# Kernel tuning notes

Hardware: AMD Instinct MI355X
Metric: run time of the kernel (lower is better)

Reference implementation:

```python
import jax, jax.numpy as jnp
import numpy as np

B, N, D, H = 16384, 64, 64, 128
DECAY_W = 2.0  # Decayer(2, 'rev') -> 1 / (1 + w * dt)
EPS = 1e-12


def setup_inputs() -> dict:
    key = jax.random.key(0)
    ks = jax.random.split(key, 16)
    return {
        "dt_node": jax.random.uniform(ks[0], (B,)) * 10.0,
        "deg_node": jax.random.uniform(ks[1], (B,)),
        "cc_node": jax.random.uniform(ks[2], (B,)),
        "dt_neigh": jax.random.uniform(ks[3], (B, N)) * 10.0,
        "deg_neigh": jax.random.uniform(ks[4], (B, N)),
        "cc_neigh": jax.random.uniform(ks[5], (B, N)),
        "neigh_mask": jax.random.bernoulli(ks[6], 0.7, (B, N)),
        "feature_hist": jax.random.normal(ks[7], (B, 2 * D)),
        "t2v_w": jax.random.normal(ks[8], (D,)) * 0.1,
        "t2v_b": jax.random.normal(ks[9], (D,)) * 0.1,
        "node_w": jax.random.normal(ks[10], (D,)) * 0.1,
        "node_b": jax.random.normal(ks[11], (D,)) * 0.1,
        "att_W1": jax.random.normal(ks[12], (D, D)) * (1.0 / np.sqrt(D)),
        "att_W2": jax.random.normal(ks[13], (D, D)) * (1.0 / np.sqrt(D)),
        "att_v": jax.random.normal(ks[14], (D,)) * (1.0 / np.sqrt(D)),
        "weight": jax.random.normal(ks[15], (H, 4 * D)) * (1.0 / np.sqrt(4 * D)),
    }


def _time2vec(t, w, b):
    # Time2Vec('cos'): first channel linear, rest cos-activated. t: [...], -> [..., D]
    v = t[..., None] * w + b
    return jnp.concatenate([v[..., :1], jnp.cos(v[..., 1:])], axis=-1)


def _node_feat(dt, deg, cc, t2v_w, t2v_b, node_w, node_b):
    # linear_node(deg) + linear_node(cc) + time2vec(|dt|), then L2 normalize
    f = (_time2vec(jnp.abs(dt), t2v_w, t2v_b)
         + (deg[..., None] * node_w + node_b)
         + (cc[..., None] * node_w + node_b))
    nrm = jnp.maximum(jnp.linalg.norm(f, axis=-1, keepdims=True), EPS)
    return f / nrm


def reference(dt_node, deg_node, cc_node, dt_neigh, deg_neigh, cc_neigh,
              neigh_mask, feature_hist, t2v_w, t2v_b, node_w, node_b,
              att_W1, att_W2, att_v, weight):
    node_f = _node_feat(dt_node, deg_node, cc_node, t2v_w, t2v_b, node_w, node_b)      # [B, D]
    neigh_f = _node_feat(dt_neigh, deg_neigh, cc_neigh, t2v_w, t2v_b, node_w, node_b)  # [B, N, D]

    # temporal decay: Decayer(2, 'rev')
    time_score = 1.0 / (1.0 + DECAY_W * dt_neigh)                                       # [B, N]

    h = jnp.tanh((node_f @ att_W1)[:, None, :] + jnp.einsum('bnd,de->bne', neigh_f, att_W2))
    att = jnp.einsum('bne,e->bn', h, att_v)                                             # [B, N]

    score = jax.nn.leaky_relu(time_score) * att                                         # [B, N]
    m = neigh_mask.astype(node_f.dtype)
    n_in = jnp.maximum(jnp.sum(m, axis=-1, keepdims=True), 1.0)                         # [B, 1]
    w_n = (m * score) / n_in                                                            # [B, N]
    neigh_agg = jnp.einsum('bn,bnd->bd', w_n, neigh_f)                                  # [B, D]

    combined = jnp.concatenate([node_f, neigh_agg, feature_hist], axis=-1)              # [B, 4D]
    return jax.nn.relu(combined @ weight.T)                                             # [B, H]
```

## Files before the change

### kernel.cpp

```cpp
#include <hip/hip_runtime.h>
#include <hip/hip_bf16.h>

#define B_SZ 16384
#define N_SZ 64
#define D_SZ 64
#define H_SZ 128
#define R_PB 4
#define ARS 68
#define CRS 264

typedef short bf16x8 __attribute__((ext_vector_type(8)));
typedef float f32x4  __attribute__((ext_vector_type(4)));
typedef float f32x2  __attribute__((ext_vector_type(2)));

__device__ __forceinline__ float bflo(unsigned u){union{unsigned i;float f;}c;c.i=u<<16;return c.f;}
__device__ __forceinline__ float bits2f(unsigned short r){union{unsigned i;float f;}c;c.i=((unsigned)r)<<16;return c.f;}
__device__ __forceinline__ unsigned f2bfbits(float f){
    __hip_bfloat16 h = __float2bfloat16(f);
    unsigned short u;
    __builtin_memcpy(&u, &h, 2);
    return (unsigned)u;
}
__device__ __forceinline__ unsigned pack2bf(float a, float b){
    __hip_bfloat162 h = __float22bfloat162_rn(make_float2(a, b));
    unsigned r;
    __builtin_memcpy(&r, &h, 4);
    return r;
}
__device__ __forceinline__ float bf2f(__hip_bfloat16 x) { return __bfloat162float(x); }

template<int CTRL>
__device__ __forceinline__ float dpp_add(float v){
    int t = __builtin_amdgcn_mov_dpp(__builtin_bit_cast(int, v), CTRL, 0xf, 0xf, true);
    return v + __builtin_bit_cast(float, t);
}

__device__ __forceinline__ float tanh_fast(float x){
    float e = __expf(2.0f * x);
    return 1.0f - __fdividef(2.0f, e + 1.0f);
}

template<int FMODE>
__device__ __forceinline__ float LD(const void* p, int i) {
    if constexpr (FMODE == 0) return bf2f(((const __hip_bfloat16*)p)[i]);
    else                      return ((const float*)p)[i];
}

__device__ __forceinline__ float mval(const void* p, int i, int mode) {
    if (mode == 0) return ((const int*)p)[i]            ? 1.0f : 0.0f;
    if (mode == 1) return ((const unsigned char*)p)[i]  ? 1.0f : 0.0f;
    if (mode == 2) return ((const unsigned short*)p)[i] ? 1.0f : 0.0f;
    return ((const unsigned int*)p)[i]                  ? 1.0f : 0.0f;
}

__device__ __forceinline__ int detect_f32(const void* p) {
    const uint4* q = (const uint4*)p;
    unsigned o = 0;
    #pragma unroll
    for (int i = 0; i < 8; ++i) { uint4 v = q[i]; o |= v.x | v.y | v.z | v.w; }
    return (o & 0x80008000u) ? 1 : 0;
}

__device__ __forceinline__ int detect_mask_mode(const void* p) {
    const uint4* q = (const uint4*)p;
    unsigned oa = 0, ofe = 0;
    #pragma unroll
    for (int i = 0; i < 8; ++i) {
        uint4 v = q[i];
        unsigned w = v.x | v.y | v.z | v.w;
        oa  |= w;
        ofe |= (v.x & 0xFEFEFEFEu) | (v.y & 0xFEFEFEFEu) | (v.z & 0xFEFEFEFEu) | (v.w & 0xFEFEFEFEu);
    }
    if ((oa & 0xFFFFFF00u) == 0) return 0;
    if (ofe == 0)                return 1;
    if (oa & 0x000000FEu)        return 2;
    return 3;
}

__global__ void prep_kernel(const void* dt_node, const void* att_W1, const void* att_W2,
                            void* ws) {
    const int t     = blockIdx.x * 256 + threadIdx.x;
    const int fmode = detect_f32(dt_node);
    const int fi  = t >> 6, ln = t & 63;
    const int et  = fi >> 2, ks = fi & 3;
    const int m16 = ln & 15, qd = ln >> 4;
    const int col = et * 16 + m16;
    unsigned short s[8];
    #pragma unroll
    for (int j = 0; j < 8; ++j) {
        const int i = ks * 32 + qd * 8 + j;
        if (fmode == 0) {
            s[j] = (i < 64) ? ((const unsigned short*)att_W1)[i * D_SZ + col]
                            : ((const unsigned short*)att_W2)[(i - 64) * D_SZ + col];
        } else {
            const float v = (i < 64) ? ((const float*)att_W1)[i * D_SZ + col]
                                     : ((const float*)att_W2)[(i - 64) * D_SZ + col];
            s[j] = (unsigned short)f2bfbits(v);
        }
    }
    ((uint4*)ws)[t] = make_uint4(((unsigned)s[0]) | (((unsigned)s[1]) << 16),
                                 ((unsigned)s[2]) | (((unsigned)s[3]) << 16),
                                 ((unsigned)s[4]) | (((unsigned)s[5]) << 16),
                                 ((unsigned)s[6]) | (((unsigned)s[7]) << 16));
}

struct Smem {
    alignas(16) unsigned short A[R_PB * 65 * ARS];
    alignas(16) unsigned short comb[R_PB * CRS];
    alignas(16) float prm[4][D_SZ];
    float att[R_PB][N_SZ];
    float wn[R_PB][N_SZ];
};

__device__ __forceinline__ void feat_row(float t, float dc,
                                         const float* sw, const float* sb,
                                         const float* snw, const float* snb,
                                         int c, unsigned short* dstA, unsigned short* dstC) {
    f32x2 fp[8]; float ss = 0.0f;
    #pragma unroll
    for (int g = 0; g < 8; ++g) {
        const f32x2 w  = *(const f32x2*)(sw  + 2 * g);
        const f32x2 b  = *(const f32x2*)(sb  + 2 * g);
        const f32x2 nw = *(const f32x2*)(snw + 2 * g);
        const f32x2 nb = *(const f32x2*)(snb + 2 * g);
        f32x2 v = w * t + b;
        f32x2 cv;
        cv.x = (c == 0 && g == 0) ? v.x : __cosf(v.x);
        cv.y = __cosf(v.y);
        f32x2 f = cv + (nw * dc + nb);
        ss = fmaf(f.x, f.x, ss);
        ss = fmaf(f.y, f.y, ss);
        fp[g] = f;
    }
    ss += __shfl_xor(ss, 1, 4);
    ss += __shfl_xor(ss, 2, 4);
    const float inv = 1.0f / fmaxf(sqrtf(ss), 1e-12f);
    unsigned pk[8];
    #pragma unroll
    for (int g = 0; g < 8; ++g)
        pk[g] = pack2bf(fp[g].x * inv, fp[g].y * inv);
    uint4 v0 = make_uint4(pk[0], pk[1], pk[2], pk[3]);
    uint4 v1 = make_uint4(pk[4], pk[5], pk[6], pk[7]);
    ((uint4*)dstA)[0] = v0; ((uint4*)dstA)[1] = v1;
    if (dstC) { ((uint4*)dstC)[0] = v0; ((uint4*)dstC)[1] = v1; }
}

template<int FMODE, bool USE_WS>
__device__ __forceinline__ void body(
    Smem& sm,
    const void* dt_node, const void* deg_node, const void* cc_node,
    const void* dt_neigh, const void* deg_neigh, const void* cc_neigh,
    const void* neigh_mask, const void* feature_hist,
    const void* t2v_w, const void* t2v_b, const void* node_w, const void* node_b,
    const void* att_W1, const void* att_W2, const void* att_v,
    const void* weight, void* out, const void* ws, int mmode, int b0, int tid)
{
    const int lane = tid & 63;
    const int wv   = tid >> 6;
    const int m16  = lane & 15;
    const int quad = lane >> 4;

    {
        const int arr = tid >> 6, ch = tid & 63;
        float v;
        if      (arr == 0) v = LD<FMODE>(t2v_w,  ch);
        else if (arr == 1) v = LD<FMODE>(t2v_b,  ch);
        else if (arr == 2) v = LD<FMODE>(node_w, ch);
        else               v = 2.0f * LD<FMODE>(node_b, ch);
        sm.prm[arr][ch] = v;
    }
    __syncthreads();

    {
        const int c = tid & 3, d0 = c * 16;
        const float* sw  = sm.prm[0] + d0;
        const float* sb  = sm.prm[1] + d0;
        const float* snw = sm.prm[2] + d0;
        const float* snb = sm.prm[3] + d0;

        #pragma unroll
        for (int it = 0; it < 5; ++it) {
            const int t = tid + it * 256;
            if (t < R_PB * 65 * 4) {
                const int f = t >> 2;
                if (f < R_PB * 64) {
                    const int row = f >> 6, n = f & 63;
                    const int idx = (b0 + row) * N_SZ + n;
                    const float tn  = fabsf(LD<FMODE>(dt_neigh, idx));
                    const float dcn = LD<FMODE>(deg_neigh, idx) + LD<FMODE>(cc_neigh, idx);
                    feat_row(tn, dcn, sw, sb, snw, snb, c,
                             sm.A + (row * 65 + n) * ARS + d0, nullptr);
                } else {
                    const int row = f - R_PB * 64;
                    const float tn = fabsf(LD<FMODE>(dt_node, b0 + row));
                    const float dc = LD<FMODE>(deg_node, b0 + row) + LD<FMODE>(cc_node, b0 + row);
                    feat_row(tn, dc, sw, sb, snw, snb, c,
                             sm.A + (row * 65 + 64) * ARS + d0,
                             sm.comb + row * CRS + d0);
                }
            }
        }
    }
    __syncthreads();

    {
        const int r = wv;
        const unsigned short* An = sm.A + (r * 65 + 64) * ARS + quad * 8;
        const bf16x8 a0 = *(const bf16x8*)An;
        const bf16x8 a1 = *(const bf16x8*)(An + 32);
        const bf16x8* wfrag = (const bf16x8*)ws;

        f32x4  accN[4];
        bf16x8 w2f[4], w3f[4];
        float  ve[4];
        #pragma unroll
        for (int et = 0; et < 4; ++et) {
            bf16x8 w0, w1;
            if constexpr (USE_WS) {
                w0      = wfrag[(et * 4 + 0) * 64 + lane];
                w1      = wfrag[(et * 4 + 1) * 64 + lane];
                w2f[et] = wfrag[(et * 4 + 2) * 64 + lane];
                w3f[et] = wfrag[(et * 4 + 3) * 64 + lane];
            } else {
                const int col = et * 16 + m16;
                #pragma unroll
                for (int j = 0; j < 8; ++j) {
                    const int k0 = quad * 8 + j;
                    if constexpr (FMODE == 0) {
                        w0[j]      = (short)((const unsigned short*)att_W1)[k0 * D_SZ + col];
                        w1[j]      = (short)((const unsigned short*)att_W1)[(k0 + 32) * D_SZ + col];
                        w2f[et][j] = (short)((const unsigned short*)att_W2)[k0 * D_SZ + col];
                        w3f[et][j] = (short)((const unsigned short*)att_W2)[(k0 + 32) * D_SZ + col];
                    } else {
                        w0[j]      = (short)f2bfbits(((const float*)att_W1)[k0 * D_SZ + col]);
                        w1[j]      = (short)f2bfbits(((const float*)att_W1)[(k0 + 32) * D_SZ + col]);
                        w2f[et][j] = (short)f2bfbits(((const float*)att_W2)[k0 * D_SZ + col]);
                        w3f[et][j] = (short)f2bfbits(((const float*)att_W2)[(k0 + 32) * D_SZ + col]);
                    }
                }
            }
            f32x4 z = {0.f, 0.f, 0.f, 0.f};
            z = __builtin_amdgcn_mfma_f32_16x16x32_bf16(a0, w0, z, 0, 0, 0);
            z = __builtin_amdgcn_mfma_f32_16x16x32_bf16(a1, w1, z, 0, 0, 0);
            accN[et] = z;
            ve[et]   = LD<FMODE>(att_v, et * 16 + m16);
        }

        #pragma unroll
        for (int mt = 0; mt < 4; ++mt) {
            const unsigned short* Ar = sm.A + (r * 65 + mt * 16 + m16) * ARS + quad * 8;
            const bf16x8 a2 = *(const bf16x8*)Ar;
            const bf16x8 a3 = *(const bf16x8*)(Ar + 32);
            float p0 = 0.f, p1 = 0.f, p2 = 0.f, p3 = 0.f;
            #pragma unroll
            for (int et = 0; et < 4; ++et) {
                f32x4 acc = __builtin_amdgcn_mfma_f32_16x16x32_bf16(a2, w2f[et], accN[et], 0, 0, 0);
                acc       = __builtin_amdgcn_mfma_f32_16x16x32_bf16(a3, w3f[et], acc,      0, 0, 0);
                p0 = fmaf(tanh_fast(acc[0]), ve[et], p0);
                p1 = fmaf(tanh_fast(acc[1]), ve[et], p1);
                p2 = fmaf(tanh_fast(acc[2]), ve[et], p2);
                p3 = fmaf(tanh_fast(acc[3]), ve[et], p3);
            }
            p0 = dpp_add<0xB1>(p0); p0 = dpp_add<0x4E>(p0); p0 = dpp_add<0x124>(p0); p0 = dpp_add<0x128>(p0);
            p1 = dpp_add<0xB1>(p1); p1 = dpp_add<0x4E>(p1); p1 = dpp_add<0x124>(p1); p1 = dpp_add<0x128>(p1);
            p2 = dpp_add<0xB1>(p2); p2 = dpp_add<0x4E>(p2); p2 = dpp_add<0x124>(p2); p2 = dpp_add<0x128>(p2);
            p3 = dpp_add<0xB1>(p3); p3 = dpp_add<0x4E>(p3); p3 = dpp_add<0x124>(p3); p3 = dpp_add<0x128>(p3);
            if (m16 == 0) {
                sm.att[r][mt * 16 + quad * 4 + 0] = p0;
                sm.att[r][mt * 16 + quad * 4 + 1] = p1;
                sm.att[r][mt * 16 + quad * 4 + 2] = p2;
                sm.att[r][mt * 16 + quad * 4 + 3] = p3;
            }
        }
    }

    {
        const int r   = wv;
        const int idx = (b0 + r) * N_SZ + lane;
        const float dt = LD<FMODE>(dt_neigh, idx);
        const float ts = 1.0f / fmaf(2.0f, dt, 1.0f);
        const float lr = ts >= 0.0f ? ts : 0.01f * ts;
        const float m  = mval(neigh_mask, idx, mmode);
        float cnt = m;
        #pragma unroll
        for (int off = 32; off > 0; off >>= 1) cnt += __shfl_down(cnt, off, 64);
        cnt = __shfl(cnt, 0, 64);
        sm.wn[r][lane] = m * lr * sm.att[r][lane] / fmaxf(cnt, 1.0f);

        if constexpr (FMODE == 0) {
            const unsigned u = ((const unsigned*)feature_hist)[(b0 + r) * 64 + lane];
            *(unsigned*)(sm.comb + r * CRS + 2 * D_SZ + 2 * lane) = u;
        } else {
            const float* fh = (const float*)feature_hist + (b0 + r) * 2 * D_SZ + 2 * lane;
            *(unsigned*)(sm.comb + r * CRS + 2 * D_SZ + 2 * lane) = pack2bf(fh[0], fh[1]);
        }
    }

    {
        const int r = wv;
        float g0 = 0.f, g1 = 0.f, g2 = 0.f, g3 = 0.f;
        #pragma unroll
        for (int n = 0; n < N_SZ; n += 4) {
            g0 = fmaf(sm.wn[r][n + 0], bits2f(sm.A[(r * 65 + n + 0) * ARS + lane]), g0);
            g1 = fmaf(sm.wn[r][n + 1], bits2f(sm.A[(r * 65 + n + 1) * ARS + lane]), g1);
            g2 = fmaf(sm.wn[r][n + 2], bits2f(sm.A[(r * 65 + n + 2) * ARS + lane]), g2);
            g3 = fmaf(sm.wn[r][n + 3], bits2f(sm.A[(r * 65 + n + 3) * ARS + lane]), g3);
        }
        const float agg = (g0 + g1) + (g2 + g3);
        sm.comb[r * CRS + D_SZ + lane] = (unsigned short)f2bfbits(agg);
    }
    __syncthreads();

    {
        #pragma unroll
        for (int t2 = 0; t2 < 2; ++t2) {
            const int nt = wv * 2 + t2;
            f32x4 c = {0.f, 0.f, 0.f, 0.f};
            #pragma unroll
            for (int ks = 0; ks < 8; ++ks) {
                const bf16x8 af = *(const bf16x8*)(sm.comb + (m16 & 3) * CRS + ks * 32 + quad * 8);
                bf16x8 bw;
                if constexpr (FMODE == 0) {
                    bw = *(const bf16x8*)((const unsigned short*)weight
                            + (nt * 16 + m16) * (4 * D_SZ) + ks * 32 + quad * 8);
                } else {
                    const float* wr = (const float*)weight
                            + (nt * 16 + m16) * (4 * D_SZ) + ks * 32 + quad * 8;
                    #pragma unroll
                    for (int j = 0; j < 8; ++j) bw[j] = (short)f2bfbits(wr[j]);
                }
                c = __builtin_amdgcn_mfma_f32_16x16x32_bf16(af, bw, c, 0, 0, 0);
            }
            if (quad == 0) {
                #pragma unroll
                for (int rr = 0; rr < R_PB; ++rr) {
                    const float v = fmaxf(c[rr], 0.0f);
                    if constexpr (FMODE == 0)
                        ((__hip_bfloat16*)out)[(b0 + rr) * H_SZ + nt * 16 + m16] = __float2bfloat16(v);
                    else
                        ((float*)out)[(b0 + rr) * H_SZ + nt * 16 + m16] = v;
                }
            }
        }
    }
}

template<bool USE_WS>
__global__ __launch_bounds__(256, 4) void fused_model_kernel(
    const void* dt_node, const void* deg_node, const void* cc_node,
    const void* dt_neigh, const void* deg_neigh, const void* cc_neigh,
    const void* neigh_mask, const void* feature_hist,
    const void* t2v_w, const void* t2v_b, const void* node_w, const void* node_b,
    const void* att_W1, const void* att_W2, const void* att_v,
    const void* weight, void* out, const void* ws)
{
    __shared__ Smem sm;
    const int b0  = blockIdx.x * R_PB;
    const int tid = threadIdx.x;

    const int fmode = __builtin_amdgcn_readfirstlane(detect_f32(dt_node));
    const int mmode = __builtin_amdgcn_readfirstlane(detect_mask_mode(neigh_mask));

    if (fmode == 0)
        body<0, USE_WS>(sm, dt_node, deg_node, cc_node, dt_neigh, deg_neigh, cc_neigh,
                        neigh_mask, feature_hist, t2v_w, t2v_b, node_w, node_b,
                        att_W1, att_W2, att_v, weight, out, ws, mmode, b0, tid);
    else
        body<1, USE_WS>(sm, dt_node, deg_node, cc_node, dt_neigh, deg_neigh, cc_neigh,
                        neigh_mask, feature_hist, t2v_w, t2v_b, node_w, node_b,
                        att_W1, att_W2, att_v, weight, out, ws, mmode, b0, tid);
}

extern "C" void kernel_launch(void* const* d_in, const int* in_sizes, int n_in,
                              void* d_out, int out_size, void* d_ws, size_t ws_size,
                              hipStream_t stream) {
    const bool use_ws = (ws_size >= 16384) && (d_ws != nullptr);
    if (use_ws) {
        prep_kernel<<<4, 256, 0, stream>>>(d_in[0], d_in[12], d_in[13], d_ws);
        fused_model_kernel<true><<<B_SZ / R_PB, 256, 0, stream>>>(
            d_in[0], d_in[1], d_in[2], d_in[3], d_in[4], d_in[5], d_in[6], d_in[7],
            d_in[8], d_in[9], d_in[10], d_in[11], d_in[12], d_in[13], d_in[14], d_in[15],
            d_out, d_ws);
    } else {
        fused_model_kernel<false><<<B_SZ / R_PB, 256, 0, stream>>>(
            d_in[0], d_in[1], d_in[2], d_in[3], d_in[4], d_in[5], d_in[6], d_in[7],
            d_in[8], d_in[9], d_in[10], d_in[11], d_in[12], d_in[13], d_in[14], d_in[15],
            d_out, d_ws);
    }
}
```

Baseline: 211.2 us.

## Use three rows per block with a dedicated wave for mask, decay and history loads

Each block now handles three batch rows instead of four. The fourth wave computes the mask, decay and count coefficients and loads the feature history in parallel with the attention MFMA waves, and the attention weight multiply moves into the aggregation loop. Cosine is evaluated with the hardware revolution-based cos by pre-scaling the t2v parameters by 1/2π, and tanh uses exp2. The cost is a ragged last block that needs clamped indices and guarded stores, a zero-padded fourth row in the final GEMM, and an extra barrier.

```diff
diff --git a/kernel.cpp b/kernel.cpp
--- a/kernel.cpp
+++ b/kernel.cpp
@@ -5,15 +5,18 @@
 #define N_SZ 64
 #define D_SZ 64
 #define H_SZ 128
-#define R_PB 4
+#define R_PB 3
 #define ARS 68
 #define CRS 264
+#define GRID ((B_SZ + R_PB - 1) / R_PB)
 
 typedef short bf16x8 __attribute__((ext_vector_type(8)));
 typedef float f32x4  __attribute__((ext_vector_type(4)));
 typedef float f32x2  __attribute__((ext_vector_type(2)));
 
-__device__ __forceinline__ float bflo(unsigned u){union{unsigned i;float f;}c;c.i=u<<16;return c.f;}
+#define INV2PI 0.15915494309189535f
+#define TWO_PI 6.283185307179586f
+
 __device__ __forceinline__ float bits2f(unsigned short r){union{unsigned i;float f;}c;c.i=((unsigned)r)<<16;return c.f;}
 __device__ __forceinline__ unsigned f2bfbits(float f){
     __hip_bfloat16 h = __float2bfloat16(f);
@@ -35,8 +38,16 @@
     return v + __builtin_bit_cast(float, t);
 }
 
+__device__ __forceinline__ float cos_rev(float v){
+#if __has_builtin(__builtin_amdgcn_cosf)
+    return __builtin_amdgcn_cosf(v - floorf(v));
+#else
+    return __cosf(v * TWO_PI);
+#endif
+}
+
 __device__ __forceinline__ float tanh_fast(float x){
-    float e = __expf(2.0f * x);
+    float e = exp2f(x * 2.8853900817779268f);
     return 1.0f - __fdividef(2.0f, e + 1.0f);
 }
 
@@ -106,10 +117,10 @@
 
 struct Smem {
     alignas(16) unsigned short A[R_PB * 65 * ARS];
-    alignas(16) unsigned short comb[R_PB * CRS];
+    alignas(16) unsigned short comb[4 * CRS];
     alignas(16) float prm[4][D_SZ];
     float att[R_PB][N_SZ];
-    float wn[R_PB][N_SZ];
+    float cf[R_PB][N_SZ];
 };
 
 __device__ __forceinline__ void feat_row(float t, float dc,
@@ -125,8 +136,8 @@
         const f32x2 nb = *(const f32x2*)(snb + 2 * g);
         f32x2 v = w * t + b;
         f32x2 cv;
-        cv.x = (c == 0 && g == 0) ? v.x : __cosf(v.x);
-        cv.y = __cosf(v.y);
+        cv.x = (c == 0 && g == 0) ? v.x * TWO_PI : cos_rev(v.x);
+        cv.y = cos_rev(v.y);
         f32x2 f = cv + (nw * dc + nb);
         ss = fmaf(f.x, f.x, ss);
         ss = fmaf(f.y, f.y, ss);
@@ -163,11 +174,12 @@
     {
         const int arr = tid >> 6, ch = tid & 63;
         float v;
-        if      (arr == 0) v = LD<FMODE>(t2v_w,  ch);
-        else if (arr == 1) v = LD<FMODE>(t2v_b,  ch);
+        if      (arr == 0) v = LD<FMODE>(t2v_w,  ch) * INV2PI;
+        else if (arr == 1) v = LD<FMODE>(t2v_b,  ch) * INV2PI;
         else if (arr == 2) v = LD<FMODE>(node_w, ch);
         else               v = 2.0f * LD<FMODE>(node_b, ch);
         sm.prm[arr][ch] = v;
+        if (tid < 128) ((unsigned*)(sm.comb + 3 * CRS))[tid] = 0;
     }
     __syncthreads();
 
@@ -179,21 +191,23 @@
         const float* snb = sm.prm[3] + d0;
 
         #pragma unroll
-        for (int it = 0; it < 5; ++it) {
+        for (int it = 0; it < 4; ++it) {
             const int t = tid + it * 256;
             if (t < R_PB * 65 * 4) {
                 const int f = t >> 2;
                 if (f < R_PB * 64) {
                     const int row = f >> 6, n = f & 63;
-                    const int idx = (b0 + row) * N_SZ + n;
+                    const int gr  = min(b0 + row, B_SZ - 1);
+                    const int idx = gr * N_SZ + n;
                     const float tn  = fabsf(LD<FMODE>(dt_neigh, idx));
                     const float dcn = LD<FMODE>(deg_neigh, idx) + LD<FMODE>(cc_neigh, idx);
                     feat_row(tn, dcn, sw, sb, snw, snb, c,
                              sm.A + (row * 65 + n) * ARS + d0, nullptr);
                 } else {
                     const int row = f - R_PB * 64;
-                    const float tn = fabsf(LD<FMODE>(dt_node, b0 + row));
-                    const float dc = LD<FMODE>(deg_node, b0 + row) + LD<FMODE>(cc_node, b0 + row);
+                    const int gr  = min(b0 + row, B_SZ - 1);
+                    const float tn = fabsf(LD<FMODE>(dt_node, gr));
+                    const float dc = LD<FMODE>(deg_node, gr) + LD<FMODE>(cc_node, gr);
                     feat_row(tn, dc, sw, sb, snw, snb, c,
                              sm.A + (row * 65 + 64) * ARS + d0,
                              sm.comb + row * CRS + d0);
@@ -203,7 +217,7 @@
     }
     __syncthreads();
 
-    {
+    if (wv < R_PB) {
         const int r = wv;
         const unsigned short* An = sm.A + (r * 65 + 64) * ARS + quad * 8;
         const bf16x8 a0 = *(const bf16x8*)An;
@@ -272,39 +286,41 @@
                 sm.att[r][mt * 16 + quad * 4 + 3] = p3;
             }
         }
-    }
-
-    {
-        const int r   = wv;
-        const int idx = (b0 + r) * N_SZ + lane;
-        const float dt = LD<FMODE>(dt_neigh, idx);
-        const float ts = 1.0f / fmaf(2.0f, dt, 1.0f);
-        const float lr = ts >= 0.0f ? ts : 0.01f * ts;
-        const float m  = mval(neigh_mask, idx, mmode);
-        float cnt = m;
-        #pragma unroll
-        for (int off = 32; off > 0; off >>= 1) cnt += __shfl_down(cnt, off, 64);
-        cnt = __shfl(cnt, 0, 64);
-        sm.wn[r][lane] = m * lr * sm.att[r][lane] / fmaxf(cnt, 1.0f);
-
-        if constexpr (FMODE == 0) {
-            const unsigned u = ((const unsigned*)feature_hist)[(b0 + r) * 64 + lane];
-            *(unsigned*)(sm.comb + r * CRS + 2 * D_SZ + 2 * lane) = u;
-        } else {
-            const float* fh = (const float*)feature_hist + (b0 + r) * 2 * D_SZ + 2 * lane;
-            *(unsigned*)(sm.comb + r * CRS + 2 * D_SZ + 2 * lane) = pack2bf(fh[0], fh[1]);
-        }
-    }
-
-    {
+    } else {
+        #pragma unroll
+        for (int r = 0; r < R_PB; ++r) {
+            const int gr  = min(b0 + r, B_SZ - 1);
+            const int idx = gr * N_SZ + lane;
+            const float dt = LD<FMODE>(dt_neigh, idx);
+            const float ts = 1.0f / fmaf(2.0f, dt, 1.0f);
+            const float lr = ts >= 0.0f ? ts : 0.01f * ts;
+            const float m  = mval(neigh_mask, idx, mmode);
+            float cnt = m;
+            #pragma unroll
+            for (int off = 32; off > 0; off >>= 1) cnt += __shfl_down(cnt, off, 64);
+            cnt = __shfl(cnt, 0, 64);
+            sm.cf[r][lane] = m * lr / fmaxf(cnt, 1.0f);
+
+            if constexpr (FMODE == 0) {
+                const unsigned u = ((const unsigned*)feature_hist)[gr * 64 + lane];
+                *(unsigned*)(sm.comb + r * CRS + 2 * D_SZ + 2 * lane) = u;
+            } else {
+                const float* fh = (const float*)feature_hist + gr * 2 * D_SZ + 2 * lane;
+                *(unsigned*)(sm.comb + r * CRS + 2 * D_SZ + 2 * lane) = pack2bf(fh[0], fh[1]);
+            }
+        }
+    }
+    __syncthreads();
+
+    if (wv < R_PB) {
         const int r = wv;
         float g0 = 0.f, g1 = 0.f, g2 = 0.f, g3 = 0.f;
         #pragma unroll
         for (int n = 0; n < N_SZ; n += 4) {
-            g0 = fmaf(sm.wn[r][n + 0], bits2f(sm.A[(r * 65 + n + 0) * ARS + lane]), g0);
-            g1 = fmaf(sm.wn[r][n + 1], bits2f(sm.A[(r * 65 + n + 1) * ARS + lane]), g1);
-            g2 = fmaf(sm.wn[r][n + 2], bits2f(sm.A[(r * 65 + n + 2) * ARS + lane]), g2);
-            g3 = fmaf(sm.wn[r][n + 3], bits2f(sm.A[(r * 65 + n + 3) * ARS + lane]), g3);
+            g0 = fmaf(sm.cf[r][n + 0] * sm.att[r][n + 0], bits2f(sm.A[(r * 65 + n + 0) * ARS + lane]), g0);
+            g1 = fmaf(sm.cf[r][n + 1] * sm.att[r][n + 1], bits2f(sm.A[(r * 65 + n + 1) * ARS + lane]), g1);
+            g2 = fmaf(sm.cf[r][n + 2] * sm.att[r][n + 2], bits2f(sm.A[(r * 65 + n + 2) * ARS + lane]), g2);
+            g3 = fmaf(sm.cf[r][n + 3] * sm.att[r][n + 3], bits2f(sm.A[(r * 65 + n + 3) * ARS + lane]), g3);
         }
         const float agg = (g0 + g1) + (g2 + g3);
         sm.comb[r * CRS + D_SZ + lane] = (unsigned short)f2bfbits(agg);
@@ -334,11 +350,13 @@
             if (quad == 0) {
                 #pragma unroll
                 for (int rr = 0; rr < R_PB; ++rr) {
-                    const float v = fmaxf(c[rr], 0.0f);
-                    if constexpr (FMODE == 0)
-                        ((__hip_bfloat16*)out)[(b0 + rr) * H_SZ + nt * 16 + m16] = __float2bfloat16(v);
-                    else
-                        ((float*)out)[(b0 + rr) * H_SZ + nt * 16 + m16] = v;
+                    if (b0 + rr < B_SZ) {
+                        const float v = fmaxf(c[rr], 0.0f);
+                        if constexpr (FMODE == 0)
+                            ((__hip_bfloat16*)out)[(b0 + rr) * H_SZ + nt * 16 + m16] = __float2bfloat16(v);
+                        else
+                            ((float*)out)[(b0 + rr) * H_SZ + nt * 16 + m16] = v;
+                    }
                 }
             }
         }
@@ -377,12 +395,12 @@
     const bool use_ws = (ws_size >= 16384) && (d_ws != nullptr);
     if (use_ws) {
         prep_kernel<<<4, 256, 0, stream>>>(d_in[0], d_in[12], d_in[13], d_ws);
-        fused_model_kernel<true><<<B_SZ / R_PB, 256, 0, stream>>>(
+        fused_model_kernel<true><<<GRID, 256, 0, stream>>>(
             d_in[0], d_in[1], d_in[2], d_in[3], d_in[4], d_in[5], d_in[6], d_in[7],
             d_in[8], d_in[9], d_in[10], d_in[11], d_in[12], d_in[13], d_in[14], d_in[15],
             d_out, d_ws);
     } else {
-        fused_model_kernel<false><<<B_SZ / R_PB, 256, 0, stream>>>(
+        fused_model_kernel<false><<<GRID, 256, 0, stream>>>(
             d_in[0], d_in[1], d_in[2], d_in[3], d_in[4], d_in[5], d_in[6], d_in[7],
             d_in[8], d_in[9], d_in[10], d_in[11], d_in[12], d_in[13], d_in[14], d_in[15],
             d_out, d_ws);
```

Measured after the change: 240.3 us. 13.8% more time.
